# Optimization experiments

Hardware: AMD Instinct MI355X
Metric: run time of the kernel (lower is better)

Reference implementation:

```python
import jax, jax.numpy as jnp
import numpy as np
import math

B, S, D = 1, 4096, 1024
H, DK = 16, 64
WINDOW = 256
GLOBAL = 16


def setup_inputs() -> dict:
    key = jax.random.key(0)
    ks = jax.random.split(key, 8)
    scale = 1.0 / math.sqrt(D)  # xavier-ish scale for projections
    return {
        "query": jax.random.normal(ks[0], (B, S, D), jnp.float32),
        "key": jax.random.normal(ks[1], (B, S, D), jnp.float32),
        "value": jax.random.normal(ks[2], (B, S, D), jnp.float32),
        "Wq": jax.random.normal(ks[3], (D, D), jnp.float32) * scale,
        "bq": jnp.zeros((D,), jnp.float32),
        "Wk": jax.random.normal(ks[4], (D, D), jnp.float32) * scale,
        "bk": jnp.zeros((D,), jnp.float32),
        "Wv": jax.random.normal(ks[5], (D, D), jnp.float32) * scale,
        "bv": jnp.zeros((D,), jnp.float32),
        "Wo": jax.random.normal(ks[6], (D, D), jnp.float32) * scale,
        "bo": jnp.zeros((D,), jnp.float32),
    }


def _split_heads(x):
    # [B, S, D] -> [B, H, S, DK]
    return x.reshape(B, S, H, DK).transpose(0, 2, 1, 3)


def reference(query, key, value, Wq, bq, Wk, bk, Wv, bv, Wo, bo):
    Q = _split_heads(query @ Wq + bq)   # [B,H,S,DK]
    K = _split_heads(key @ Wk + bk)
    V = _split_heads(value @ Wv + bv)

    scores = jnp.einsum("bhqd,bhkd->bhqk", Q, K) / math.sqrt(DK)  # [B,H,S,S]

    i = jnp.arange(S)[:, None]
    j = jnp.arange(S)[None, :]
    local = jnp.abs(i - j) <= WINDOW
    glob = (i < GLOBAL) | (j < GLOBAL)
    causal = j <= i
    mask = (local | glob) & causal  # [S,S]

    scores = jnp.where(mask[None, None], scores, -jnp.inf)
    probs = jax.nn.softmax(scores, axis=-1)  # dropout is identity (p=0 / eval)

    out = jnp.einsum("bhqk,bhkd->bhqd", probs, V)  # [B,H,S,DK]
    out = out.transpose(0, 2, 1, 3).reshape(B, S, D)
    return out @ Wo + bo
```

## Files before the change

kernel.cpp:

```cpp
#include <hip/hip_runtime.h>

typedef __bf16 bf16_t;
typedef __attribute__((ext_vector_type(8))) __bf16 bf16x8;
typedef __attribute__((ext_vector_type(4))) __bf16 bf16x4;
typedef __attribute__((ext_vector_type(2))) __bf16 bf16x2;
typedef __attribute__((ext_vector_type(4))) float f32x4;

#define S_LEN 4096
#define D_MODEL 1024
#define NH 16
#define DKH 64
#define WIN 256
#define NGLOB 16
#define HSZ (S_LEN * DKH)

__device__ inline void g2l16(const void* g, void* l) {
  __builtin_amdgcn_global_load_lds(
      (__attribute__((address_space(1))) void*)(void*)g,
      (__attribute__((address_space(3))) void*)l, 16, 0, 0);
}

template <bool AF32>
__device__ __forceinline__ void gemm_body(const void* __restrict__ Ap,
                                          const bf16_t* __restrict__ Bt,
                                          int m0, int n0, int wave, int lane,
                                          bf16_t* As, bf16_t* Bs,
                                          f32x4 acc[4][4]) {
  const float* Af = (const float*)Ap;
  const bf16_t* Ah = (const bf16_t*)Ap;
  const int wr = wave >> 1, wc = wave & 1;
#pragma unroll
  for (int i = 0; i < 4; i++)
#pragma unroll
    for (int j = 0; j < 4; j++) acc[i][j] = {0.f, 0.f, 0.f, 0.f};

  const int ssl = (lane & 7) ^ (lane >> 3);
  const int srowB = 2 * (lane >> 3) + (ssl >> 2);
  const int scolB = 8 * (ssl & 3);
  const int arow_l = lane >> 2;
  const int aslot = lane & 3;
  const int fr = lane & 15;
  const int fkg = lane >> 4;

#define A_LDS_OFF(c)                                                        \
  ((((c)*16 + arow_l) >> 1) * 64 +                                          \
   (((((c)*16 + arow_l) & 1) << 2 | aslot) ^ ((((c)*16 + arow_l) >> 1) & 7)) * 8)

  for (int k0 = 0; k0 < D_MODEL; k0 += 32) {
#pragma unroll
    for (int i = 0; i < 2; i++) {
      const int c = wave * 2 + i;
      g2l16(Bt + (size_t)(n0 + c * 16 + srowB) * D_MODEL + k0 + scolB,
            &Bs[c * 512]);
    }
    if constexpr (AF32) {
      const int c0 = wave * 2, c1 = wave * 2 + 1;
      const float* s0 =
          Af + (size_t)(m0 + c0 * 16 + arow_l) * D_MODEL + k0 + aslot * 8;
      const float* s1 =
          Af + (size_t)(m0 + c1 * 16 + arow_l) * D_MODEL + k0 + aslot * 8;
      const float4 x0 = *(const float4*)s0;
      const float4 y0 = *(const float4*)(s0 + 4);
      const float4 x1 = *(const float4*)s1;
      const float4 y1 = *(const float4*)(s1 + 4);
      *(bf16x8*)&As[A_LDS_OFF(c0)] =
          bf16x8{(bf16_t)x0.x, (bf16_t)x0.y, (bf16_t)x0.z, (bf16_t)x0.w,
                 (bf16_t)y0.x, (bf16_t)y0.y, (bf16_t)y0.z, (bf16_t)y0.w};
      *(bf16x8*)&As[A_LDS_OFF(c1)] =
          bf16x8{(bf16_t)x1.x, (bf16_t)x1.y, (bf16_t)x1.z, (bf16_t)x1.w,
                 (bf16_t)y1.x, (bf16_t)y1.y, (bf16_t)y1.z, (bf16_t)y1.w};
    } else {
#pragma unroll
      for (int i = 0; i < 2; i++) {
        const int c = wave * 2 + i;
        g2l16(Ah + (size_t)(m0 + c * 16 + srowB) * D_MODEL + k0 + scolB,
              &As[c * 512]);
      }
    }
    __syncthreads();
    bf16x8 af[4], bfr[4];
#pragma unroll
    for (int m = 0; m < 4; m++) {
      const int rr = wr * 64 + m * 16 + fr;
      af[m] = *(const bf16x8*)&As[(rr >> 1) * 64 +
                                  ((((rr & 1) << 2) + fkg) ^ ((rr >> 1) & 7)) *
                                      8];
    }
#pragma unroll
    for (int n = 0; n < 4; n++) {
      const int rr = wc * 64 + n * 16 + fr;
      bfr[n] = *(const bf16x8*)&Bs[(rr >> 1) * 64 +
                                   ((((rr & 1) << 2) + fkg) ^ ((rr >> 1) & 7)) *
                                       8];
    }
#pragma unroll
    for (int m = 0; m < 4; m++)
#pragma unroll
      for (int n = 0; n < 4; n++)
        acc[m][n] = __builtin_amdgcn_mfma_f32_16x16x32_bf16(af[m], bfr[n],
                                                            acc[m][n], 0, 0, 0);
    __syncthreads();
  }
#undef A_LDS_OFF
}

__global__ __launch_bounds__(256) void gemm_qkv(
    const float* __restrict__ Xq, const float* __restrict__ Xk,
    const float* __restrict__ Xv, const bf16_t* __restrict__ Wt,
    const float* __restrict__ bq, const float* __restrict__ bk,
    const float* __restrict__ bv, bf16_t* __restrict__ Qo,
    bf16_t* __restrict__ Ko, bf16_t* __restrict__ Vto) {
  __shared__ bf16_t As[128 * 32];
  __shared__ bf16_t Bs[128 * 32];
  const int lin = blockIdx.x;
  const int wg = ((lin & 7) * 96) + (lin >> 3);
  const int n0 = (wg & 7) * 128;
  const int m0 = ((wg >> 3) & 31) * 128;
  const int which = wg >> 8;

  const float* A = which == 0 ? Xq : which == 1 ? Xk : Xv;
  const bf16_t* Bt = Wt + (size_t)which * (D_MODEL * D_MODEL);
  const float* bias = which == 0 ? bq : which == 1 ? bk : bv;

  const int wave = threadIdx.x >> 6, lane = threadIdx.x & 63;
  f32x4 acc[4][4];
  gemm_body<true>(A, Bt, m0, n0, wave, lane, As, Bs, acc);

  const int wr = wave >> 1, wc = wave & 1;
  const int cr = (lane >> 4) * 4;
  const int cc = lane & 15;
#pragma unroll
  for (int m = 0; m < 4; m++) {
    const int rowg = m0 + wr * 64 + m * 16 + cr;
#pragma unroll
    for (int n = 0; n < 4; n++) {
      const int colg = n0 + wc * 64 + n * 16 + cc;
      const float bv_ = bias[colg];
      const int h = colg >> 6, d = colg & 63;
#pragma unroll
      for (int r = 0; r < 4; r++) {
        const int s = rowg + r;
        const float v = acc[m][n][r] + bv_;
        if (which == 0)
          Qo[h * HSZ + s * DKH + d] = (bf16_t)(v * 0.125f);
        else if (which == 1)
          Ko[h * HSZ + s * DKH + d] = (bf16_t)v;
        else
          Vto[h * HSZ + d * S_LEN + s] = (bf16_t)v;
      }
    }
  }
}

__global__ __launch_bounds__(256) void gemm_out(const bf16_t* __restrict__ A_,
                                                const bf16_t* __restrict__ Bt_,
                                                const float* __restrict__ bias,
                                                float* __restrict__ Cout) {
  __shared__ bf16_t As[128 * 32];
  __shared__ bf16_t Bs[128 * 32];
  const int lin = blockIdx.x;
  const int wg = ((lin & 7) * 32) + (lin >> 3);
  const int n0 = (wg & 7) * 128;
  const int m0 = (wg >> 3) * 128;
  const int wave = threadIdx.x >> 6, lane = threadIdx.x & 63;
  f32x4 acc[4][4];
  gemm_body<false>(A_, Bt_, m0, n0, wave, lane, As, Bs, acc);

  const int wr = wave >> 1, wc = wave & 1;
  const int cr = (lane >> 4) * 4;
  const int cc = lane & 15;
#pragma unroll
  for (int m = 0; m < 4; m++) {
    const int rowg = m0 + wr * 64 + m * 16 + cr;
#pragma unroll
    for (int n = 0; n < 4; n++) {
      const int colg = n0 + wc * 64 + n * 16 + cc;
      const float bv_ = bias[colg];
#pragma unroll
      for (int r = 0; r < 4; r++)
        Cout[(size_t)(rowg + r) * D_MODEL + colg] = acc[m][n][r] + bv_;
    }
  }
}

__global__ void convw(const float* __restrict__ W0, const float* __restrict__ W1,
                      const float* __restrict__ W2, const float* __restrict__ W3,
                      bf16_t* __restrict__ out) {
  __shared__ float t[64][65];
  const float* W = blockIdx.z == 0 ? W0 : blockIdx.z == 1 ? W1
                  : blockIdx.z == 2 ? W2 : W3;
  bf16_t* Wt = out + (size_t)blockIdx.z * (D_MODEL * D_MODEL);
  const int k0 = blockIdx.y * 64, n0 = blockIdx.x * 64;
  const int tx = threadIdx.x & 63, ty = threadIdx.x >> 6;
#pragma unroll
  for (int i = 0; i < 16; i++) {
    const int r = i * 4 + ty;
    t[r][tx] = W[(size_t)(k0 + r) * D_MODEL + n0 + tx];
  }
  __syncthreads();
#pragma unroll
  for (int i = 0; i < 16; i++) {
    const int r = i * 4 + ty;
    Wt[(size_t)(n0 + r) * D_MODEL + k0 + tx] = (bf16_t)t[tx][r];
  }
}

__global__ __launch_bounds__(256) void attn_kern(const bf16_t* __restrict__ Q,
                                                 const bf16_t* __restrict__ K,
                                                 const bf16_t* __restrict__ V,
                                                 bf16_t* __restrict__ O) {
  __shared__ bf16_t p_lds[4][16 * 40];
  const int wave = threadIdx.x >> 6, lane = threadIdx.x & 63;
  const int h = blockIdx.y;
  const int q0 = blockIdx.x * 64 + wave * 16;
  const bf16_t* Qh = Q + h * HSZ;
  const bf16_t* Kh = K + h * HSZ;
  const bf16_t* Vh = V + h * HSZ;

  const int fr = lane & 15;
  const int fk = (lane >> 4) * 8;
  const int cr = (lane >> 4) * 4;

  const bf16x8 aq0 = *(const bf16x8*)&Qh[(q0 + fr) * DKH + fk];
  const bf16x8 aq1 = *(const bf16x8*)&Qh[(q0 + fr) * DKH + 32 + fk];

  f32x4 acc_o[4];
#pragma unroll
  for (int i = 0; i < 4; i++) acc_o[i] = {0.f, 0.f, 0.f, 0.f};
  float m_run = -1e30f, l_run = 0.f;

  const int kt_end = (q0 + 15) >> 5;
  int kt_lo = (q0 - WIN) >> 5;
  if (kt_lo < 0) kt_lo = 0;
  const int nt = kt_end - kt_lo + 1 + (kt_lo > 0 ? 1 : 0);

#define TILE_KB(t) ((kt_lo > 0) ? ((t) == 0 ? 0 : (kt_lo + (t)-1) * 32) : (t)*32)
#define LOADK(kb, A0, A1, A2, A3)                              \
  A0 = *(const bf16x8*)&Kh[((kb) + fr) * DKH + fk];            \
  A1 = *(const bf16x8*)&Kh[((kb) + fr) * DKH + 32 + fk];       \
  A2 = *(const bf16x8*)&Kh[((kb) + 16 + fr) * DKH + fk];       \
  A3 = *(const bf16x8*)&Kh[((kb) + 16 + fr) * DKH + 32 + fk];

  bf16x8 kc0, kc1, kc2, kc3;
  {
    const int kb0 = TILE_KB(0);
    LOADK(kb0, kc0, kc1, kc2, kc3)
  }

  const int iq = q0 + fr;
  bf16_t* prow = &p_lds[wave][fr * 40];
  const bf16x8* pread = (const bf16x8*)&p_lds[wave][fr * 40 + fk];

  for (int t = 0; t < nt; t++) {
    const int kb = TILE_KB(t);
    bf16x8 kn0, kn1, kn2, kn3;
    const bool have_next = (t + 1 < nt);
    if (have_next) {
      const int nkb = TILE_KB(t + 1);
      LOADK(nkb, kn0, kn1, kn2, kn3)
    }
    bf16x8 vf0 = *(const bf16x8*)&Vh[(0 * 16 + fr) * S_LEN + kb + fk];
    bf16x8 vf1 = *(const bf16x8*)&Vh[(1 * 16 + fr) * S_LEN + kb + fk];
    bf16x8 vf2 = *(const bf16x8*)&Vh[(2 * 16 + fr) * S_LEN + kb + fk];
    bf16x8 vf3 = *(const bf16x8*)&Vh[(3 * 16 + fr) * S_LEN + kb + fk];

    f32x4 s0 = {0.f, 0.f, 0.f, 0.f}, s1 = {0.f, 0.f, 0.f, 0.f};
    s0 = __builtin_amdgcn_mfma_f32_16x16x32_bf16(kc0, aq0, s0, 0, 0, 0);
    s0 = __builtin_amdgcn_mfma_f32_16x16x32_bf16(kc1, aq1, s0, 0, 0, 0);
    s1 = __builtin_amdgcn_mfma_f32_16x16x32_bf16(kc2, aq0, s1, 0, 0, 0);
    s1 = __builtin_amdgcn_mfma_f32_16x16x32_bf16(kc3, aq1, s1, 0, 0, 0);

    float v[8];
#pragma unroll
    for (int r = 0; r < 4; r++) {
      const int j0 = kb + cr + r, j1 = j0 + 16;
      v[r] = (j0 <= iq && (iq - j0 <= WIN || j0 < NGLOB)) ? s0[r] : -1e30f;
      v[4 + r] = (j1 <= iq && (iq - j1 <= WIN || j1 < NGLOB)) ? s1[r] : -1e30f;
    }
    float mt = fmaxf(fmaxf(fmaxf(v[0], v[1]), fmaxf(v[2], v[3])),
                     fmaxf(fmaxf(v[4], v[5]), fmaxf(v[6], v[7])));
    mt = fmaxf(mt, __shfl_xor(mt, 16));
    mt = fmaxf(mt, __shfl_xor(mt, 32));
    const float mn = fmaxf(m_run, mt);
    const float alpha = __expf(m_run - mn);
    m_run = mn;
    float p[8];
    float ps = 0.f;
#pragma unroll
    for (int i = 0; i < 8; i++) {
      p[i] = __expf(v[i] - mn);
      ps += p[i];
    }
    ps += __shfl_xor(ps, 16);
    ps += __shfl_xor(ps, 32);
    l_run = l_run * alpha + ps;

    *(bf16x2*)&prow[cr] = bf16x2{(bf16_t)p[0], (bf16_t)p[1]};
    *(bf16x2*)&prow[cr + 2] = bf16x2{(bf16_t)p[2], (bf16_t)p[3]};
    *(bf16x2*)&prow[16 + cr] = bf16x2{(bf16_t)p[4], (bf16_t)p[5]};
    *(bf16x2*)&prow[16 + cr + 2] = bf16x2{(bf16_t)p[6], (bf16_t)p[7]};

    float alpha_r[4];
#pragma unroll
    for (int r = 0; r < 4; r++) alpha_r[r] = __shfl(alpha, cr + r);

    asm volatile("" ::: "memory");
    const bf16x8 pa = *pread;
    asm volatile("" ::: "memory");

#pragma unroll
    for (int fd = 0; fd < 4; fd++) {
#pragma unroll
      for (int r = 0; r < 4; r++) acc_o[fd][r] *= alpha_r[r];
    }
    acc_o[0] = __builtin_amdgcn_mfma_f32_16x16x32_bf16(pa, vf0, acc_o[0], 0, 0, 0);
    acc_o[1] = __builtin_amdgcn_mfma_f32_16x16x32_bf16(pa, vf1, acc_o[1], 0, 0, 0);
    acc_o[2] = __builtin_amdgcn_mfma_f32_16x16x32_bf16(pa, vf2, acc_o[2], 0, 0, 0);
    acc_o[3] = __builtin_amdgcn_mfma_f32_16x16x32_bf16(pa, vf3, acc_o[3], 0, 0, 0);

    if (have_next) {
      kc0 = kn0; kc1 = kn1; kc2 = kn2; kc3 = kn3;
    }
  }

  const float linv = 1.0f / l_run;
  float inv_r[4];
#pragma unroll
  for (int r = 0; r < 4; r++) inv_r[r] = __shfl(linv, cr + r);

#pragma unroll
  for (int fd = 0; fd < 4; fd++)
#pragma unroll
    for (int r = 0; r < 4; r++) {
      const int s = q0 + cr + r;
      O[(size_t)s * D_MODEL + h * DKH + fd * 16 + fr] =
          (bf16_t)(acc_o[fd][r] * inv_r[r]);
    }
}

extern "C" void kernel_launch(void* const* d_in, const int* in_sizes, int n_in,
                              void* d_out, int out_size, void* d_ws,
                              size_t ws_size, hipStream_t stream) {
  const float* query = (const float*)d_in[0];
  const float* key = (const float*)d_in[1];
  const float* value = (const float*)d_in[2];
  const float* Wq = (const float*)d_in[3];
  const float* bq = (const float*)d_in[4];
  const float* Wk = (const float*)d_in[5];
  const float* bk = (const float*)d_in[6];
  const float* Wv = (const float*)d_in[7];
  const float* bv = (const float*)d_in[8];
  const float* Wo = (const float*)d_in[9];
  const float* bo = (const float*)d_in[10];

  char* ws = (char*)d_ws;
  bf16_t* Qb = (bf16_t*)(ws);
  bf16_t* Kb = (bf16_t*)(ws + (8ull << 20));
  bf16_t* Vtb = (bf16_t*)(ws + (16ull << 20));
  bf16_t* Wt = (bf16_t*)(ws + (24ull << 20));
  bf16_t* Ab = (bf16_t*)(ws + (32ull << 20));

  const size_t WSTRIDE = (size_t)D_MODEL * D_MODEL;

  convw<<<dim3(16, 16, 4), 256, 0, stream>>>(Wq, Wk, Wv, Wo, Wt);

  gemm_qkv<<<768, 256, 0, stream>>>(query, key, value, Wt, bq, bk, bv, Qb, Kb,
                                    Vtb);

  attn_kern<<<dim3(64, 16), 256, 0, stream>>>(Qb, Kb, Vtb, Ab);

  gemm_out<<<256, 256, 0, stream>>>(Ab, Wt + 3 * WSTRIDE, bo, (float*)d_out);
}
```

Baseline: 131.8 us.

## Double-buffer LDS tiles in QKV and output projection GEMMs

Rewrites the shared GEMM mainloop as a two-stage pipeline. The next K-slice is prefetched into a second LDS buffer while MFMAs run on the current one, and there is now one barrier per iteration instead of two. For fp32 A inputs, the global loads are issued early and converted to bf16 and stored to LDS after the MFMAs, which hides load latency. LDS per block doubles, which can lower occupancy, and holding the prefetched values raises register pressure.

```diff
diff --git a/kernel.cpp b/kernel.cpp
--- a/kernel.cpp
+++ b/kernel.cpp
@@ -20,8 +20,12 @@
       (__attribute__((address_space(3))) void*)l, 16, 0, 0);
 }
 
+#define A_LDS_OFF(c)                                                        \
+  ((((c)*16 + arow_l) >> 1) * 64 +                                          \
+   (((((c)*16 + arow_l) & 1) << 2 | aslot) ^ ((((c)*16 + arow_l) >> 1) & 7)) * 8)
+
 template <bool AF32>
-__device__ __forceinline__ void gemm_body(const void* __restrict__ Ap,
+__device__ __forceinline__ void gemm_pipe(const void* __restrict__ Ap,
                                           const bf16_t* __restrict__ Bt,
                                           int m0, int n0, int wave, int lane,
                                           bf16_t* As, bf16_t* Bs,
@@ -42,54 +46,71 @@
   const int fr = lane & 15;
   const int fkg = lane >> 4;
 
-#define A_LDS_OFF(c)                                                        \
-  ((((c)*16 + arow_l) >> 1) * 64 +                                          \
-   (((((c)*16 + arow_l) & 1) << 2 | aslot) ^ ((((c)*16 + arow_l) >> 1) & 7)) * 8)
-
-  for (int k0 = 0; k0 < D_MODEL; k0 += 32) {
-#pragma unroll
-    for (int i = 0; i < 2; i++) {
-      const int c = wave * 2 + i;
-      g2l16(Bt + (size_t)(n0 + c * 16 + srowB) * D_MODEL + k0 + scolB,
-            &Bs[c * 512]);
-    }
-    if constexpr (AF32) {
-      const int c0 = wave * 2, c1 = wave * 2 + 1;
-      const float* s0 =
-          Af + (size_t)(m0 + c0 * 16 + arow_l) * D_MODEL + k0 + aslot * 8;
-      const float* s1 =
-          Af + (size_t)(m0 + c1 * 16 + arow_l) * D_MODEL + k0 + aslot * 8;
-      const float4 x0 = *(const float4*)s0;
-      const float4 y0 = *(const float4*)(s0 + 4);
-      const float4 x1 = *(const float4*)s1;
-      const float4 y1 = *(const float4*)(s1 + 4);
-      *(bf16x8*)&As[A_LDS_OFF(c0)] =
-          bf16x8{(bf16_t)x0.x, (bf16_t)x0.y, (bf16_t)x0.z, (bf16_t)x0.w,
-                 (bf16_t)y0.x, (bf16_t)y0.y, (bf16_t)y0.z, (bf16_t)y0.w};
-      *(bf16x8*)&As[A_LDS_OFF(c1)] =
-          bf16x8{(bf16_t)x1.x, (bf16_t)x1.y, (bf16_t)x1.z, (bf16_t)x1.w,
-                 (bf16_t)y1.x, (bf16_t)y1.y, (bf16_t)y1.z, (bf16_t)y1.w};
-    } else {
-#pragma unroll
-      for (int i = 0; i < 2; i++) {
-        const int c = wave * 2 + i;
-        g2l16(Ah + (size_t)(m0 + c * 16 + srowB) * D_MODEL + k0 + scolB,
-              &As[c * 512]);
+  const int c0 = wave * 2, c1 = wave * 2 + 1;
+
+  g2l16(Bt + (size_t)(n0 + c0 * 16 + srowB) * D_MODEL + scolB, &Bs[c0 * 512]);
+  g2l16(Bt + (size_t)(n0 + c1 * 16 + srowB) * D_MODEL + scolB, &Bs[c1 * 512]);
+  if constexpr (AF32) {
+    const float* s0 = Af + (size_t)(m0 + c0 * 16 + arow_l) * D_MODEL + aslot * 8;
+    const float* s1 = Af + (size_t)(m0 + c1 * 16 + arow_l) * D_MODEL + aslot * 8;
+    const float4 x0 = *(const float4*)s0;
+    const float4 y0 = *(const float4*)(s0 + 4);
+    const float4 x1 = *(const float4*)s1;
+    const float4 y1 = *(const float4*)(s1 + 4);
+    *(bf16x8*)&As[A_LDS_OFF(c0)] =
+        bf16x8{(bf16_t)x0.x, (bf16_t)x0.y, (bf16_t)x0.z, (bf16_t)x0.w,
+               (bf16_t)y0.x, (bf16_t)y0.y, (bf16_t)y0.z, (bf16_t)y0.w};
+    *(bf16x8*)&As[A_LDS_OFF(c1)] =
+        bf16x8{(bf16_t)x1.x, (bf16_t)x1.y, (bf16_t)x1.z, (bf16_t)x1.w,
+               (bf16_t)y1.x, (bf16_t)y1.y, (bf16_t)y1.z, (bf16_t)y1.w};
+  } else {
+    g2l16(Ah + (size_t)(m0 + c0 * 16 + srowB) * D_MODEL + scolB, &As[c0 * 512]);
+    g2l16(Ah + (size_t)(m0 + c1 * 16 + srowB) * D_MODEL + scolB, &As[c1 * 512]);
+  }
+
+#pragma unroll 2
+  for (int t = 0; t < 32; ++t) {
+    const int cur = (t & 1) * 4096;
+    const int nxt = ((t + 1) & 1) * 4096;
+    __syncthreads();
+
+    const bool hn = (t + 1 < 32);
+    float4 ax0{}, ay0{}, ax1{}, ay1{};
+    if (hn) {
+      const int kn = (t + 1) * 32;
+      g2l16(Bt + (size_t)(n0 + c0 * 16 + srowB) * D_MODEL + kn + scolB,
+            &Bs[nxt + c0 * 512]);
+      g2l16(Bt + (size_t)(n0 + c1 * 16 + srowB) * D_MODEL + kn + scolB,
+            &Bs[nxt + c1 * 512]);
+      if constexpr (AF32) {
+        const float* s0 =
+            Af + (size_t)(m0 + c0 * 16 + arow_l) * D_MODEL + kn + aslot * 8;
+        const float* s1 =
+            Af + (size_t)(m0 + c1 * 16 + arow_l) * D_MODEL + kn + aslot * 8;
+        ax0 = *(const float4*)s0;
+        ay0 = *(const float4*)(s0 + 4);
+        ax1 = *(const float4*)s1;
+        ay1 = *(const float4*)(s1 + 4);
+      } else {
+        g2l16(Ah + (size_t)(m0 + c0 * 16 + srowB) * D_MODEL + kn + scolB,
+              &As[nxt + c0 * 512]);
+        g2l16(Ah + (size_t)(m0 + c1 * 16 + srowB) * D_MODEL + kn + scolB,
+              &As[nxt + c1 * 512]);
       }
     }
-    __syncthreads();
+
     bf16x8 af[4], bfr[4];
 #pragma unroll
     for (int m = 0; m < 4; m++) {
       const int rr = wr * 64 + m * 16 + fr;
-      af[m] = *(const bf16x8*)&As[(rr >> 1) * 64 +
+      af[m] = *(const bf16x8*)&As[cur + (rr >> 1) * 64 +
                                   ((((rr & 1) << 2) + fkg) ^ ((rr >> 1) & 7)) *
                                       8];
     }
 #pragma unroll
     for (int n = 0; n < 4; n++) {
       const int rr = wc * 64 + n * 16 + fr;
-      bfr[n] = *(const bf16x8*)&Bs[(rr >> 1) * 64 +
+      bfr[n] = *(const bf16x8*)&Bs[cur + (rr >> 1) * 64 +
                                    ((((rr & 1) << 2) + fkg) ^ ((rr >> 1) & 7)) *
                                        8];
     }
@@ -99,9 +120,18 @@
       for (int n = 0; n < 4; n++)
         acc[m][n] = __builtin_amdgcn_mfma_f32_16x16x32_bf16(af[m], bfr[n],
                                                             acc[m][n], 0, 0, 0);
-    __syncthreads();
-  }
-#undef A_LDS_OFF
+
+    if (hn) {
+      if constexpr (AF32) {
+        *(bf16x8*)&As[nxt + A_LDS_OFF(c0)] =
+            bf16x8{(bf16_t)ax0.x, (bf16_t)ax0.y, (bf16_t)ax0.z, (bf16_t)ax0.w,
+                   (bf16_t)ay0.x, (bf16_t)ay0.y, (bf16_t)ay0.z, (bf16_t)ay0.w};
+        *(bf16x8*)&As[nxt + A_LDS_OFF(c1)] =
+            bf16x8{(bf16_t)ax1.x, (bf16_t)ax1.y, (bf16_t)ax1.z, (bf16_t)ax1.w,
+                   (bf16_t)ay1.x, (bf16_t)ay1.y, (bf16_t)ay1.z, (bf16_t)ay1.w};
+      }
+    }
+  }
 }
 
 __global__ __launch_bounds__(256) void gemm_qkv(
@@ -110,8 +140,8 @@
     const float* __restrict__ bq, const float* __restrict__ bk,
     const float* __restrict__ bv, bf16_t* __restrict__ Qo,
     bf16_t* __restrict__ Ko, bf16_t* __restrict__ Vto) {
-  __shared__ bf16_t As[128 * 32];
-  __shared__ bf16_t Bs[128 * 32];
+  __shared__ bf16_t As[2 * 128 * 32];
+  __shared__ bf16_t Bs[2 * 128 * 32];
   const int lin = blockIdx.x;
   const int wg = ((lin & 7) * 96) + (lin >> 3);
   const int n0 = (wg & 7) * 128;
@@ -124,7 +154,7 @@
 
   const int wave = threadIdx.x >> 6, lane = threadIdx.x & 63;
   f32x4 acc[4][4];
-  gemm_body<true>(A, Bt, m0, n0, wave, lane, As, Bs, acc);
+  gemm_pipe<true>(A, Bt, m0, n0, wave, lane, As, Bs, acc);
 
   const int wr = wave >> 1, wc = wave & 1;
   const int cr = (lane >> 4) * 4;
@@ -156,15 +186,15 @@
                                                 const bf16_t* __restrict__ Bt_,
                                                 const float* __restrict__ bias,
                                                 float* __restrict__ Cout) {
-  __shared__ bf16_t As[128 * 32];
-  __shared__ bf16_t Bs[128 * 32];
+  __shared__ bf16_t As[2 * 128 * 32];
+  __shared__ bf16_t Bs[2 * 128 * 32];
   const int lin = blockIdx.x;
   const int wg = ((lin & 7) * 32) + (lin >> 3);
   const int n0 = (wg & 7) * 128;
   const int m0 = (wg >> 3) * 128;
   const int wave = threadIdx.x >> 6, lane = threadIdx.x & 63;
   f32x4 acc[4][4];
-  gemm_body<false>(A_, Bt_, m0, n0, wave, lane, As, Bs, acc);
+  gemm_pipe<false>(A_, Bt_, m0, n0, wave, lane, As, Bs, acc);
 
   const int wr = wave >> 1, wc = wave & 1;
   const int cr = (lane >> 4) * 4;
```

New measurement: 159.8 us. +21.2%, slower.

## Widen attention key tiles to 64 and add MFMA priority hints

Applied to the files above, without the earlier changes.

The attention loop now walks keys in 64-wide tiles instead of 32-wide ones. This halves the number of online-softmax iterations, along with their shuffles, exp rescales and LDS round-trips. The explicit register prefetch of the next K tile is removed in favour of loading K and V at the top of each iteration, and s_setprio is raised around the MFMA groups. Wider tiles do more masked-out work at the window edges and use more registers, and dropping the prefetch may expose load latency.

```diff
diff --git a/kernel.cpp b/kernel.cpp
--- a/kernel.cpp
+++ b/kernel.cpp
@@ -19,6 +19,10 @@
       (__attribute__((address_space(1))) void*)(void*)g,
       (__attribute__((address_space(3))) void*)l, 16, 0, 0);
 }
+
+#define A_LDS_OFF(c)                                                        \
+  ((((c)*16 + arow_l) >> 1) * 64 +                                          \
+   (((((c)*16 + arow_l) & 1) << 2 | aslot) ^ ((((c)*16 + arow_l) >> 1) & 7)) * 8)
 
 template <bool AF32>
 __device__ __forceinline__ void gemm_body(const void* __restrict__ Ap,
@@ -41,10 +45,6 @@
   const int aslot = lane & 3;
   const int fr = lane & 15;
   const int fkg = lane >> 4;
-
-#define A_LDS_OFF(c)                                                        \
-  ((((c)*16 + arow_l) >> 1) * 64 +                                          \
-   (((((c)*16 + arow_l) & 1) << 2 | aslot) ^ ((((c)*16 + arow_l) >> 1) & 7)) * 8)
 
   for (int k0 = 0; k0 < D_MODEL; k0 += 32) {
 #pragma unroll
@@ -101,7 +101,6 @@
                                                             acc[m][n], 0, 0, 0);
     __syncthreads();
   }
-#undef A_LDS_OFF
 }
 
 __global__ __launch_bounds__(256) void gemm_qkv(
@@ -209,7 +208,7 @@
                                                  const bf16_t* __restrict__ K,
                                                  const bf16_t* __restrict__ V,
                                                  bf16_t* __restrict__ O) {
-  __shared__ bf16_t p_lds[4][16 * 40];
+  __shared__ bf16_t p_lds[4][16 * 72];
   const int wave = threadIdx.x >> 6, lane = threadIdx.x & 63;
   const int h = blockIdx.y;
   const int q0 = blockIdx.x * 64 + wave * 16;
@@ -229,65 +228,66 @@
   for (int i = 0; i < 4; i++) acc_o[i] = {0.f, 0.f, 0.f, 0.f};
   float m_run = -1e30f, l_run = 0.f;
 
-  const int kt_end = (q0 + 15) >> 5;
-  int kt_lo = (q0 - WIN) >> 5;
+  const int kt_end = (q0 + 15) >> 6;
+  int kt_lo = (q0 - WIN) >> 6;
   if (kt_lo < 0) kt_lo = 0;
   const int nt = kt_end - kt_lo + 1 + (kt_lo > 0 ? 1 : 0);
 
-#define TILE_KB(t) ((kt_lo > 0) ? ((t) == 0 ? 0 : (kt_lo + (t)-1) * 32) : (t)*32)
-#define LOADK(kb, A0, A1, A2, A3)                              \
-  A0 = *(const bf16x8*)&Kh[((kb) + fr) * DKH + fk];            \
-  A1 = *(const bf16x8*)&Kh[((kb) + fr) * DKH + 32 + fk];       \
-  A2 = *(const bf16x8*)&Kh[((kb) + 16 + fr) * DKH + fk];       \
-  A3 = *(const bf16x8*)&Kh[((kb) + 16 + fr) * DKH + 32 + fk];
-
-  bf16x8 kc0, kc1, kc2, kc3;
-  {
-    const int kb0 = TILE_KB(0);
-    LOADK(kb0, kc0, kc1, kc2, kc3)
-  }
-
   const int iq = q0 + fr;
-  bf16_t* prow = &p_lds[wave][fr * 40];
-  const bf16x8* pread = (const bf16x8*)&p_lds[wave][fr * 40 + fk];
+  bf16_t* prow = &p_lds[wave][fr * 72];
+  const bf16_t* prd = &p_lds[wave][fr * 72];
 
   for (int t = 0; t < nt; t++) {
-    const int kb = TILE_KB(t);
-    bf16x8 kn0, kn1, kn2, kn3;
-    const bool have_next = (t + 1 < nt);
-    if (have_next) {
-      const int nkb = TILE_KB(t + 1);
-      LOADK(nkb, kn0, kn1, kn2, kn3)
-    }
-    bf16x8 vf0 = *(const bf16x8*)&Vh[(0 * 16 + fr) * S_LEN + kb + fk];
-    bf16x8 vf1 = *(const bf16x8*)&Vh[(1 * 16 + fr) * S_LEN + kb + fk];
-    bf16x8 vf2 = *(const bf16x8*)&Vh[(2 * 16 + fr) * S_LEN + kb + fk];
-    bf16x8 vf3 = *(const bf16x8*)&Vh[(3 * 16 + fr) * S_LEN + kb + fk];
-
-    f32x4 s0 = {0.f, 0.f, 0.f, 0.f}, s1 = {0.f, 0.f, 0.f, 0.f};
-    s0 = __builtin_amdgcn_mfma_f32_16x16x32_bf16(kc0, aq0, s0, 0, 0, 0);
-    s0 = __builtin_amdgcn_mfma_f32_16x16x32_bf16(kc1, aq1, s0, 0, 0, 0);
-    s1 = __builtin_amdgcn_mfma_f32_16x16x32_bf16(kc2, aq0, s1, 0, 0, 0);
-    s1 = __builtin_amdgcn_mfma_f32_16x16x32_bf16(kc3, aq1, s1, 0, 0, 0);
-
-    float v[8];
-#pragma unroll
-    for (int r = 0; r < 4; r++) {
-      const int j0 = kb + cr + r, j1 = j0 + 16;
-      v[r] = (j0 <= iq && (iq - j0 <= WIN || j0 < NGLOB)) ? s0[r] : -1e30f;
-      v[4 + r] = (j1 <= iq && (iq - j1 <= WIN || j1 < NGLOB)) ? s1[r] : -1e30f;
-    }
-    float mt = fmaxf(fmaxf(fmaxf(v[0], v[1]), fmaxf(v[2], v[3])),
-                     fmaxf(fmaxf(v[4], v[5]), fmaxf(v[6], v[7])));
+    const int kt = (kt_lo > 0) ? (t == 0 ? 0 : kt_lo + t - 1) : t;
+    const int kb = kt * 64;
+
+    bf16x8 kc[4][2];
+#pragma unroll
+    for (int j = 0; j < 4; j++) {
+      kc[j][0] = *(const bf16x8*)&Kh[(kb + 16 * j + fr) * DKH + fk];
+      kc[j][1] = *(const bf16x8*)&Kh[(kb + 16 * j + fr) * DKH + 32 + fk];
+    }
+    bf16x8 vf[4][2];
+#pragma unroll
+    for (int fd = 0; fd < 4; fd++) {
+      vf[fd][0] = *(const bf16x8*)&Vh[(fd * 16 + fr) * S_LEN + kb + fk];
+      vf[fd][1] = *(const bf16x8*)&Vh[(fd * 16 + fr) * S_LEN + kb + 32 + fk];
+    }
+
+    f32x4 s[4];
+#pragma unroll
+    for (int j = 0; j < 4; j++) s[j] = {0.f, 0.f, 0.f, 0.f};
+    __builtin_amdgcn_s_setprio(1);
+#pragma unroll
+    for (int j = 0; j < 4; j++) {
+      s[j] = __builtin_amdgcn_mfma_f32_16x16x32_bf16(kc[j][0], aq0, s[j], 0, 0, 0);
+      s[j] = __builtin_amdgcn_mfma_f32_16x16x32_bf16(kc[j][1], aq1, s[j], 0, 0, 0);
+    }
+    __builtin_amdgcn_s_setprio(0);
+
+    float v[16];
+#pragma unroll
+    for (int j = 0; j < 4; j++)
+#pragma unroll
+      for (int r = 0; r < 4; r++) {
+        const int jj = kb + 16 * j + cr + r;
+        v[4 * j + r] =
+            (jj <= iq && (iq - jj <= WIN || jj < NGLOB)) ? s[j][r] : -1e30f;
+      }
+    float m01 = fmaxf(fmaxf(v[0], v[1]), fmaxf(v[2], v[3]));
+    float m23 = fmaxf(fmaxf(v[4], v[5]), fmaxf(v[6], v[7]));
+    float m45 = fmaxf(fmaxf(v[8], v[9]), fmaxf(v[10], v[11]));
+    float m67 = fmaxf(fmaxf(v[12], v[13]), fmaxf(v[14], v[15]));
+    float mt = fmaxf(fmaxf(m01, m23), fmaxf(m45, m67));
     mt = fmaxf(mt, __shfl_xor(mt, 16));
     mt = fmaxf(mt, __shfl_xor(mt, 32));
     const float mn = fmaxf(m_run, mt);
     const float alpha = __expf(m_run - mn);
     m_run = mn;
-    float p[8];
+    float p[16];
     float ps = 0.f;
 #pragma unroll
-    for (int i = 0; i < 8; i++) {
+    for (int i = 0; i < 16; i++) {
       p[i] = __expf(v[i] - mn);
       ps += p[i];
     }
@@ -295,17 +295,20 @@
     ps += __shfl_xor(ps, 32);
     l_run = l_run * alpha + ps;
 
-    *(bf16x2*)&prow[cr] = bf16x2{(bf16_t)p[0], (bf16_t)p[1]};
-    *(bf16x2*)&prow[cr + 2] = bf16x2{(bf16_t)p[2], (bf16_t)p[3]};
-    *(bf16x2*)&prow[16 + cr] = bf16x2{(bf16_t)p[4], (bf16_t)p[5]};
-    *(bf16x2*)&prow[16 + cr + 2] = bf16x2{(bf16_t)p[6], (bf16_t)p[7]};
+#pragma unroll
+    for (int j = 0; j < 4; j++) {
+      *(bf16x2*)&prow[16 * j + cr] = bf16x2{(bf16_t)p[4 * j], (bf16_t)p[4 * j + 1]};
+      *(bf16x2*)&prow[16 * j + cr + 2] =
+          bf16x2{(bf16_t)p[4 * j + 2], (bf16_t)p[4 * j + 3]};
+    }
 
     float alpha_r[4];
 #pragma unroll
     for (int r = 0; r < 4; r++) alpha_r[r] = __shfl(alpha, cr + r);
 
     asm volatile("" ::: "memory");
-    const bf16x8 pa = *pread;
+    const bf16x8 pa0 = *(const bf16x8*)&prd[fk];
+    const bf16x8 pa1 = *(const bf16x8*)&prd[32 + fk];
     asm volatile("" ::: "memory");
 
 #pragma unroll
@@ -313,14 +316,15 @@
 #pragma unroll
       for (int r = 0; r < 4; r++) acc_o[fd][r] *= alpha_r[r];
     }
-    acc_o[0] = __builtin_amdgcn_mfma_f32_16x16x32_bf16(pa, vf0, acc_o[0], 0, 0, 0);
-    acc_o[1] = __builtin_amdgcn_mfma_f32_16x16x32_bf16(pa, vf1, acc_o[1], 0, 0, 0);
-    acc_o[2] = __builtin_amdgcn_mfma_f32_16x16x32_bf16(pa, vf2, acc_o[2], 0, 0, 0);
-    acc_o[3] = __builtin_amdgcn_mfma_f32_16x16x32_bf16(pa, vf3, acc_o[3], 0, 0, 0);
-
-    if (have_next) {
-      kc0 = kn0; kc1 = kn1; kc2 = kn2; kc3 = kn3;
-    }
+    __builtin_amdgcn_s_setprio(1);
+#pragma unroll
+    for (int fd = 0; fd < 4; fd++) {
+      acc_o[fd] =
+          __builtin_amdgcn_mfma_f32_16x16x32_bf16(pa0, vf[fd][0], acc_o[fd], 0, 0, 0);
+      acc_o[fd] =
+          __builtin_amdgcn_mfma_f32_16x16x32_bf16(pa1, vf[fd][1], acc_o[fd], 0, 0, 0);
+    }
+    __builtin_amdgcn_s_setprio(0);
   }
 
   const float linv = 1.0f / l_run;
```

New measurement: 139.8 us. 1.06x slower.

## Pre-convert activations to bf16 in a merged conversion kernel and remap attention blocks

Applied to the files above, without the earlier changes.

Adds a combined conversion kernel that casts the fp32 query/key/value inputs to bf16 in workspace alongside the weight transpose. The QKV GEMM then loads A tiles asynchronously into LDS like the B tiles, instead of doing fp32 loads plus register conversion inside the main loop. The attention launch becomes 1D with an XCD-aware block remap so neighbouring heads and blocks share caches. In exchange it adds an extra full read and write pass over the activations (about 48MB fp32 read, 24MB bf16 written) before the GEMM.

```diff
diff --git a/kernel.cpp b/kernel.cpp
--- a/kernel.cpp
+++ b/kernel.cpp
@@ -20,14 +20,11 @@
       (__attribute__((address_space(3))) void*)l, 16, 0, 0);
 }
 
-template <bool AF32>
-__device__ __forceinline__ void gemm_body(const void* __restrict__ Ap,
+__device__ __forceinline__ void gemm_body(const bf16_t* __restrict__ Ah,
                                           const bf16_t* __restrict__ Bt,
                                           int m0, int n0, int wave, int lane,
                                           bf16_t* As, bf16_t* Bs,
                                           f32x4 acc[4][4]) {
-  const float* Af = (const float*)Ap;
-  const bf16_t* Ah = (const bf16_t*)Ap;
   const int wr = wave >> 1, wc = wave & 1;
 #pragma unroll
   for (int i = 0; i < 4; i++)
@@ -37,14 +34,8 @@
   const int ssl = (lane & 7) ^ (lane >> 3);
   const int srowB = 2 * (lane >> 3) + (ssl >> 2);
   const int scolB = 8 * (ssl & 3);
-  const int arow_l = lane >> 2;
-  const int aslot = lane & 3;
   const int fr = lane & 15;
   const int fkg = lane >> 4;
-
-#define A_LDS_OFF(c)                                                        \
-  ((((c)*16 + arow_l) >> 1) * 64 +                                          \
-   (((((c)*16 + arow_l) & 1) << 2 | aslot) ^ ((((c)*16 + arow_l) >> 1) & 7)) * 8)
 
   for (int k0 = 0; k0 < D_MODEL; k0 += 32) {
 #pragma unroll
@@ -52,30 +43,8 @@
       const int c = wave * 2 + i;
       g2l16(Bt + (size_t)(n0 + c * 16 + srowB) * D_MODEL + k0 + scolB,
             &Bs[c * 512]);
-    }
-    if constexpr (AF32) {
-      const int c0 = wave * 2, c1 = wave * 2 + 1;
-      const float* s0 =
-          Af + (size_t)(m0 + c0 * 16 + arow_l) * D_MODEL + k0 + aslot * 8;
-      const float* s1 =
-          Af + (size_t)(m0 + c1 * 16 + arow_l) * D_MODEL + k0 + aslot * 8;
-      const float4 x0 = *(const float4*)s0;
-      const float4 y0 = *(const float4*)(s0 + 4);
-      const float4 x1 = *(const float4*)s1;
-      const float4 y1 = *(const float4*)(s1 + 4);
-      *(bf16x8*)&As[A_LDS_OFF(c0)] =
-          bf16x8{(bf16_t)x0.x, (bf16_t)x0.y, (bf16_t)x0.z, (bf16_t)x0.w,
-                 (bf16_t)y0.x, (bf16_t)y0.y, (bf16_t)y0.z, (bf16_t)y0.w};
-      *(bf16x8*)&As[A_LDS_OFF(c1)] =
-          bf16x8{(bf16_t)x1.x, (bf16_t)x1.y, (bf16_t)x1.z, (bf16_t)x1.w,
-                 (bf16_t)y1.x, (bf16_t)y1.y, (bf16_t)y1.z, (bf16_t)y1.w};
-    } else {
-#pragma unroll
-      for (int i = 0; i < 2; i++) {
-        const int c = wave * 2 + i;
-        g2l16(Ah + (size_t)(m0 + c * 16 + srowB) * D_MODEL + k0 + scolB,
-              &As[c * 512]);
-      }
+      g2l16(Ah + (size_t)(m0 + c * 16 + srowB) * D_MODEL + k0 + scolB,
+            &As[c * 512]);
     }
     __syncthreads();
     bf16x8 af[4], bfr[4];
@@ -101,12 +70,11 @@
                                                             acc[m][n], 0, 0, 0);
     __syncthreads();
   }
-#undef A_LDS_OFF
 }
 
 __global__ __launch_bounds__(256) void gemm_qkv(
-    const float* __restrict__ Xq, const float* __restrict__ Xk,
-    const float* __restrict__ Xv, const bf16_t* __restrict__ Wt,
+    const bf16_t* __restrict__ Xq, const bf16_t* __restrict__ Xk,
+    const bf16_t* __restrict__ Xv, const bf16_t* __restrict__ Wt,
     const float* __restrict__ bq, const float* __restrict__ bk,
     const float* __restrict__ bv, bf16_t* __restrict__ Qo,
     bf16_t* __restrict__ Ko, bf16_t* __restrict__ Vto) {
@@ -118,13 +86,13 @@
   const int m0 = ((wg >> 3) & 31) * 128;
   const int which = wg >> 8;
 
-  const float* A = which == 0 ? Xq : which == 1 ? Xk : Xv;
+  const bf16_t* A = which == 0 ? Xq : which == 1 ? Xk : Xv;
   const bf16_t* Bt = Wt + (size_t)which * (D_MODEL * D_MODEL);
   const float* bias = which == 0 ? bq : which == 1 ? bk : bv;
 
   const int wave = threadIdx.x >> 6, lane = threadIdx.x & 63;
   f32x4 acc[4][4];
-  gemm_body<true>(A, Bt, m0, n0, wave, lane, As, Bs, acc);
+  gemm_body(A, Bt, m0, n0, wave, lane, As, Bs, acc);
 
   const int wr = wave >> 1, wc = wave & 1;
   const int cr = (lane >> 4) * 4;
@@ -164,7 +132,7 @@
   const int m0 = (wg >> 3) * 128;
   const int wave = threadIdx.x >> 6, lane = threadIdx.x & 63;
   f32x4 acc[4][4];
-  gemm_body<false>(A_, Bt_, m0, n0, wave, lane, As, Bs, acc);
+  gemm_body(A_, Bt_, m0, n0, wave, lane, As, Bs, acc);
 
   const int wr = wave >> 1, wc = wave & 1;
   const int cr = (lane >> 4) * 4;
@@ -183,25 +151,43 @@
   }
 }
 
-__global__ void convw(const float* __restrict__ W0, const float* __restrict__ W1,
-                      const float* __restrict__ W2, const float* __restrict__ W3,
-                      bf16_t* __restrict__ out) {
+__global__ __launch_bounds__(256) void conv_all(
+    const float* __restrict__ q, const float* __restrict__ k,
+    const float* __restrict__ v, const float* __restrict__ W0,
+    const float* __restrict__ W1, const float* __restrict__ W2,
+    const float* __restrict__ W3, bf16_t* __restrict__ oq,
+    bf16_t* __restrict__ ok, bf16_t* __restrict__ ov,
+    bf16_t* __restrict__ Wt) {
   __shared__ float t[64][65];
-  const float* W = blockIdx.z == 0 ? W0 : blockIdx.z == 1 ? W1
-                  : blockIdx.z == 2 ? W2 : W3;
-  bf16_t* Wt = out + (size_t)blockIdx.z * (D_MODEL * D_MODEL);
-  const int k0 = blockIdx.y * 64, n0 = blockIdx.x * 64;
-  const int tx = threadIdx.x & 63, ty = threadIdx.x >> 6;
-#pragma unroll
-  for (int i = 0; i < 16; i++) {
-    const int r = i * 4 + ty;
-    t[r][tx] = W[(size_t)(k0 + r) * D_MODEL + n0 + tx];
-  }
-  __syncthreads();
-#pragma unroll
-  for (int i = 0; i < 16; i++) {
-    const int r = i * 4 + ty;
-    Wt[(size_t)(n0 + r) * D_MODEL + k0 + tx] = (bf16_t)t[tx][r];
+  const int bid = blockIdx.x;
+  if (bid < 12288) {
+    const int which = bid >> 12;
+    const int blk = bid & 4095;
+    const float* in = which == 0 ? q : which == 1 ? k : v;
+    bf16_t* out = which == 0 ? oq : which == 1 ? ok : ov;
+    const int i = (blk * 256 + threadIdx.x) * 4;
+    const float4 x = *(const float4*)&in[i];
+    bf16x4 o = {(bf16_t)x.x, (bf16_t)x.y, (bf16_t)x.z, (bf16_t)x.w};
+    *(bf16x4*)&out[i] = o;
+  } else {
+    const int wb = bid - 12288;
+    const int wz = wb >> 8;
+    const int rem = wb & 255;
+    const float* W = wz == 0 ? W0 : wz == 1 ? W1 : wz == 2 ? W2 : W3;
+    bf16_t* Wo = Wt + (size_t)wz * (D_MODEL * D_MODEL);
+    const int k0 = (rem >> 4) * 64, n0 = (rem & 15) * 64;
+    const int tx = threadIdx.x & 63, ty = threadIdx.x >> 6;
+#pragma unroll
+    for (int i = 0; i < 16; i++) {
+      const int r = i * 4 + ty;
+      t[r][tx] = W[(size_t)(k0 + r) * D_MODEL + n0 + tx];
+    }
+    __syncthreads();
+#pragma unroll
+    for (int i = 0; i < 16; i++) {
+      const int r = i * 4 + ty;
+      Wo[(size_t)(n0 + r) * D_MODEL + k0 + tx] = (bf16_t)t[tx][r];
+    }
   }
 }
 
@@ -211,8 +197,10 @@
                                                  bf16_t* __restrict__ O) {
   __shared__ bf16_t p_lds[4][16 * 40];
   const int wave = threadIdx.x >> 6, lane = threadIdx.x & 63;
-  const int h = blockIdx.y;
-  const int q0 = blockIdx.x * 64 + wave * 16;
+  const int lin = blockIdx.x;
+  const int wg = (lin & 7) * 128 + (lin >> 3);
+  const int h = wg >> 6;
+  const int q0 = (wg & 63) * 64 + wave * 16;
   const bf16_t* Qh = Q + h * HSZ;
   const bf16_t* Kh = K + h * HSZ;
   const bf16_t* Vh = V + h * HSZ;
@@ -358,16 +346,19 @@
   bf16_t* Kb = (bf16_t*)(ws + (8ull << 20));
   bf16_t* Vtb = (bf16_t*)(ws + (16ull << 20));
   bf16_t* Wt = (bf16_t*)(ws + (24ull << 20));
-  bf16_t* Ab = (bf16_t*)(ws + (32ull << 20));
+  bf16_t* Xq = (bf16_t*)(ws + (32ull << 20));
+  bf16_t* Xk = (bf16_t*)(ws + (40ull << 20));
+  bf16_t* Xv = (bf16_t*)(ws + (48ull << 20));
+  bf16_t* Ab = (bf16_t*)(ws + (56ull << 20));
 
   const size_t WSTRIDE = (size_t)D_MODEL * D_MODEL;
 
-  convw<<<dim3(16, 16, 4), 256, 0, stream>>>(Wq, Wk, Wv, Wo, Wt);
-
-  gemm_qkv<<<768, 256, 0, stream>>>(query, key, value, Wt, bq, bk, bv, Qb, Kb,
-                                    Vtb);
-
-  attn_kern<<<dim3(64, 16), 256, 0, stream>>>(Qb, Kb, Vtb, Ab);
+  conv_all<<<13312, 256, 0, stream>>>(query, key, value, Wq, Wk, Wv, Wo, Xq,
+                                      Xk, Xv, Wt);
+
+  gemm_qkv<<<768, 256, 0, stream>>>(Xq, Xk, Xv, Wt, bq, bk, bv, Qb, Kb, Vtb);
+
+  attn_kern<<<1024, 256, 0, stream>>>(Qb, Kb, Vtb, Ab);
 
   gemm_out<<<256, 256, 0, stream>>>(Ab, Wt + 3 * WSTRIDE, bo, (float*)d_out);
 }
```

After: 132.2 us. About the same (+0.2%).
